# Optimization experiments

Hardware: AMD Instinct MI355X
Metric: run time of the kernel (lower is better)

## Reference

```python
import jax, jax.numpy as jnp
import numpy as np

IN_CAPS, IN_DIM, OUT_CAPS, OUT_DIM = 2048, 8, 32, 16
NUM_ROUTING = 3
EPS = 1e-9


def squash(s):
    # s: [..., out_dim]
    s2 = jnp.sum(s * s, axis=-1, keepdims=True)
    return (s2 / (1.0 + s2)) * (s / jnp.sqrt(s2 + EPS))


def setup_inputs() -> dict:
    key = jax.random.key(0)
    kx, kw = jax.random.split(key)
    x = jax.random.normal(kx, (64, IN_CAPS, IN_DIM), dtype=jnp.float32)
    W = jax.random.normal(kw, (1, IN_CAPS, OUT_CAPS, OUT_DIM, IN_DIM), dtype=jnp.float32) * 0.01
    return {"x": x, "W": W}


def reference(x, W):
    # u_hat[b,i,o,j] = sum_d W[0,i,o,j,d] * x[b,i,d]
    u_hat = jnp.einsum('iojd,bid->bioj', W[0], x)  # [B, in_caps, out_caps, out_dim]
    b_ij = jnp.zeros(u_hat.shape[:3], dtype=u_hat.dtype)  # [B, in_caps, out_caps]
    v_j = None
    for r in range(NUM_ROUTING):
        c_ij = jax.nn.softmax(b_ij, axis=2)[..., None]  # [B, in, out, 1]
        s_j = jnp.sum(c_ij * u_hat, axis=1)             # [B, out, out_dim]
        v_j = squash(s_j)
        if r < NUM_ROUTING - 1:
            b_ij = b_ij + jnp.einsum('bioj,boj->bio', u_hat, v_j)
    return v_j
```

## Files before the change

kernel.cpp:

```cpp
#include <hip/hip_runtime.h>
#include <math.h>


#define IC 2048
#define ID 8
#define OC 32
#define OD 16
#define B_N 64
#define S_ELEMS (B_N * OC * OD)
#define IB 16
#define ISTR (IC / IB)
#define BPB 16
#define BG (B_N / BPB)

__device__ __forceinline__ void gll16(const float4* g, float4* l)
{
    __builtin_amdgcn_global_load_lds(
        (const __attribute__((address_space(1))) void*)g,
        (__attribute__((address_space(3))) void*)l,
        16, 0, 0);
}

template <int CTRL>
__device__ __forceinline__ float dpp_add(float x)
{
    union { float f; int i; } a, b;
    a.f = x;
    b.i = __builtin_amdgcn_update_dpp(0, a.i, CTRL, 0xF, 0xF, true);
    return x + b.f;
}


template <int FIRST>
__launch_bounds__(256, 2)
__global__ void caps_pass(const float* __restrict__ Wg,
                          const float* __restrict__ xg,
                          const float* __restrict__ vs,
                          float* __restrict__ part)
{
    __shared__ float4 Wl[4][1024];
    __shared__ float4 xs[BPB * 32];

    const int tid  = threadIdx.x;
    const int lane = tid & 63;
    const int w    = tid >> 6;
    const int o    = lane & 31;
    const int jh   = lane >> 5;

    const int is   = blockIdx.x & (ISTR - 1);
    const int bg   = blockIdx.x >> 7;
    const int bblk = bg * BPB;
    const int ig0  = is * IB;

    const float4* wq = (const float4*)Wg;
    const float4* xq = (const float4*)xg;

    float4 va[4], vb[4];
    if (!FIRST) {
#pragma unroll
        for (int n = 0; n < 4; ++n) {
            const float* vp =
                vs + (size_t)(bblk + w * 4 + n) * (OC * OD) + o * OD + jh * 8;
            va[n] = ((const float4*)vp)[0];
            vb[n] = ((const float4*)vp)[1];
        }
    }

    float acc[4][8];
#pragma unroll
    for (int n = 0; n < 4; ++n)
#pragma unroll
        for (int jj = 0; jj < 8; ++jj) acc[n][jj] = 0.0f;

    auto stage = [&](int t) {
        const size_t wb0 = (size_t)(ig0 + t) * 1024;
        float4* dst = Wl[t & 3];
#pragma unroll
        for (int s = 0; s < 4; ++s) {
            const int D = s * 256 + tid;
            const int orow = D >> 5;
            const int f = orow * 32 + ((D & 31) ^ orow);
            gll16(wq + wb0 + f, dst + D);
        }
    };

    stage(0);
    stage(1);
    {
#pragma unroll
        for (int q = 0; q < 2; ++q) {
            const int s = q * 256 + tid;
            const int b = s >> 5;
            const int r = s & 31;
            gll16(xq + ((size_t)(bblk + b) * IC + ig0) * 2 + r, &xs[s]);
        }
    }

    auto compute = [&](int il) {
        float4 wA[8], wB[8];
        const float4* buf = Wl[il & 3];
        const int row = o * 32;
#pragma unroll
        for (int jj = 0; jj < 8; ++jj) {
            const int ca = (jh * 16 + jj * 2) ^ o;
            wA[jj] = buf[row + ca];
            wB[jj] = buf[row + (ca ^ 1)];
        }

#pragma unroll
        for (int n = 0; n < 4; ++n) {
            const float4 xa = xs[(w * 4 + n) * 32 + il * 2];
            const float4 xb = xs[(w * 4 + n) * 32 + il * 2 + 1];
            float u[8];
#pragma unroll
            for (int jj = 0; jj < 8; ++jj) {
                float t = wA[jj].x * xa.x;
                t = fmaf(wA[jj].y, xa.y, t);
                t = fmaf(wA[jj].z, xa.z, t);
                t = fmaf(wA[jj].w, xa.w, t);
                t = fmaf(wB[jj].x, xb.x, t);
                t = fmaf(wB[jj].y, xb.y, t);
                t = fmaf(wB[jj].z, xb.z, t);
                t = fmaf(wB[jj].w, xb.w, t);
                u[jj] = t;
            }
            float cc;
            if (FIRST) {
                cc = 1.0f;
            } else {
                float bp = u[0] * va[n].x;
                bp = fmaf(u[1], va[n].y, bp);
                bp = fmaf(u[2], va[n].z, bp);
                bp = fmaf(u[3], va[n].w, bp);
                bp = fmaf(u[4], vb[n].x, bp);
                bp = fmaf(u[5], vb[n].y, bp);
                bp = fmaf(u[6], vb[n].z, bp);
                bp = fmaf(u[7], vb[n].w, bp);
                bp += __shfl_xor(bp, 32);
                const float e = __expf(bp);
                float t = dpp_add<0xB1>(e);
                t = dpp_add<0x4E>(t);
                t = dpp_add<0x124>(t);
                t = dpp_add<0x128>(t);
                const float se = t + __shfl_xor(t, 16);
                cc = e * __builtin_amdgcn_rcpf(se);
            }
#pragma unroll
            for (int jj = 0; jj < 8; ++jj)
                acc[n][jj] = fmaf(cc, u[jj], acc[n][jj]);
        }
    };

    for (int il = 0; il < IB - 2; ++il) {
        stage(il + 2);
        asm volatile("s_waitcnt vmcnt(8)" ::: "memory");
        __builtin_amdgcn_s_barrier();
        compute(il);
    }
    asm volatile("s_waitcnt vmcnt(4)" ::: "memory");
    __builtin_amdgcn_s_barrier();
    compute(IB - 2);
    asm volatile("s_waitcnt vmcnt(0)" ::: "memory");
    __builtin_amdgcn_s_barrier();
    compute(IB - 1);

    const float scale = FIRST ? (1.0f / 32.0f) : 1.0f;
#pragma unroll
    for (int n = 0; n < 4; ++n) {
        float* dst = part + (size_t)is * S_ELEMS
                   + (size_t)(bblk + w * 4 + n) * (OC * OD) + o * OD + jh * 8;
        float4 lo = {acc[n][0] * scale, acc[n][1] * scale,
                     acc[n][2] * scale, acc[n][3] * scale};
        float4 hi = {acc[n][4] * scale, acc[n][5] * scale,
                     acc[n][6] * scale, acc[n][7] * scale};
        ((float4*)dst)[0] = lo;
        ((float4*)dst)[1] = hi;
    }
}

template <int MODE>
__launch_bounds__(256, 4)
__global__ void caps_reduce(const float* __restrict__ part,
                            float* __restrict__ vsum,
                            float* __restrict__ out)
{
    __shared__ float red[4][64];
    const int tid  = threadIdx.x;
    const int w    = tid >> 6;
    const int lane = tid & 63;
    const int e0   = blockIdx.x * 64;

    float s = 0.0f;
#pragma unroll 8
    for (int k = w; k < ISTR; k += 4)
        s += part[(size_t)k * S_ELEMS + e0 + lane];
    red[w][lane] = s;
    __syncthreads();

    if (tid < 64) {
        const float t = red[0][tid] + red[1][tid] + red[2][tid] + red[3][tid];
        float s2 = t * t;
        s2 += __shfl_xor(s2, 1);
        s2 += __shfl_xor(s2, 2);
        s2 += __shfl_xor(s2, 4);
        s2 += __shfl_xor(s2, 8);
        const float v = t * (s2 / ((1.0f + s2) * sqrtf(s2 + 1e-9f)));
        const int e = e0 + tid;
        if (MODE == 0)      vsum[e] = v;
        else if (MODE == 1) vsum[e] += v;
        else                out[e] = v;
    }
}

extern "C" void kernel_launch(void* const* d_in, const int* in_sizes, int n_in,
                              void* d_out, int out_size, void* d_ws, size_t ws_size,
                              hipStream_t stream)
{
    const float* x = (const float*)d_in[0];
    const float* W = (const float*)d_in[1];
    float* out = (float*)d_out;

    float* part = (float*)d_ws;
    float* vsum = part + (size_t)ISTR * S_ELEMS;

    const dim3 gP(BG * ISTR);
    const dim3 bP(256);
    const dim3 gR(S_ELEMS / 64);
    const dim3 bR(256);

    caps_pass<1><<<gP, bP, 0, stream>>>(W, x, nullptr, part);
    caps_reduce<0><<<gR, bR, 0, stream>>>(part, vsum, out);
    caps_pass<0><<<gP, bP, 0, stream>>>(W, x, vsum, part);
    caps_reduce<1><<<gR, bR, 0, stream>>>(part, vsum, out);
    caps_pass<0><<<gP, bP, 0, stream>>>(W, x, vsum, part);
    caps_reduce<2><<<gR, bR, 0, stream>>>(part, vsum, out);
}
```

Before: 170.2 us.

## Fuse all routing passes and reductions into one persistent kernel with grid barriers

Merges the three routing passes and three reduction kernels into a single kernel launch. Atomic-counter grid barriers separate each pass from its reduction, which removes five launch gaps and the kernel boundaries between them. The W pipeline shrinks from a 4-deep async ring to double buffering with __syncthreads, which may expose more load latency. The design assumes all 512 blocks are co-resident (2 per CU over 256 CUs); without that the barrier deadlocks. It also adds a memset launch per call.

New measurement: 537.2 us. +215.7%, slower.

```diff
diff --git a/kernel.cpp b/kernel.cpp
--- a/kernel.cpp
+++ b/kernel.cpp
@@ -12,6 +12,7 @@
 #define ISTR (IC / IB)
 #define BPB 16
 #define BG (B_N / BPB)
+#define NBLK (BG * ISTR)
 
 __device__ __forceinline__ void gll16(const float4* g, float4* l)
 {
@@ -30,16 +31,44 @@
     return x + b.f;
 }
 
-
-template <int FIRST>
+__device__ __forceinline__ void gridbar(unsigned* cnt, unsigned* gen)
+{
+    __syncthreads();
+    if (threadIdx.x == 0) {
+        const unsigned g =
+            __hip_atomic_load(gen, __ATOMIC_RELAXED, __HIP_MEMORY_SCOPE_AGENT);
+        const unsigned a =
+            __hip_atomic_fetch_add(cnt, 1u, __ATOMIC_ACQ_REL,
+                                   __HIP_MEMORY_SCOPE_AGENT);
+        if (a == NBLK - 1) {
+            __hip_atomic_store(cnt, 0u, __ATOMIC_RELAXED,
+                               __HIP_MEMORY_SCOPE_AGENT);
+            __hip_atomic_fetch_add(gen, 1u, __ATOMIC_RELEASE,
+                                   __HIP_MEMORY_SCOPE_AGENT);
+        } else {
+            while (__hip_atomic_load(gen, __ATOMIC_ACQUIRE,
+                                     __HIP_MEMORY_SCOPE_AGENT) == g)
+                __builtin_amdgcn_s_sleep(2);
+        }
+    }
+    __syncthreads();
+}
+
+
 __launch_bounds__(256, 2)
-__global__ void caps_pass(const float* __restrict__ Wg,
-                          const float* __restrict__ xg,
-                          const float* __restrict__ vs,
-                          float* __restrict__ part)
-{
-    __shared__ float4 Wl[4][1024];
-    __shared__ float4 xs[BPB * 32];
+__global__ void caps_fused(const float* __restrict__ Wg,
+                           const float* __restrict__ xg,
+                           float* __restrict__ part,
+                           float* __restrict__ vsum,
+                           float* __restrict__ out,
+                           unsigned* __restrict__ bar)
+{
+    __shared__ float4 Wl[2][1024];
+    __shared__ float4 xs[BPB * 2 * IB];
+    __shared__ float red[4][64];
+
+    unsigned* cnt = bar;
+    unsigned* gen = bar + 1;
 
     const int tid  = threadIdx.x;
     const int lane = tid & 63;
@@ -51,164 +80,148 @@
     const int bg   = blockIdx.x >> 7;
     const int bblk = bg * BPB;
     const int ig0  = is * IB;
+    const int e0   = blockIdx.x * 64;
 
     const float4* wq = (const float4*)Wg;
     const float4* xq = (const float4*)xg;
 
-    float4 va[4], vb[4];
-    if (!FIRST) {
-#pragma unroll
-        for (int n = 0; n < 4; ++n) {
-            const float* vp =
-                vs + (size_t)(bblk + w * 4 + n) * (OC * OD) + o * OD + jh * 8;
-            va[n] = ((const float4*)vp)[0];
-            vb[n] = ((const float4*)vp)[1];
-        }
+#pragma unroll
+    for (int q = 0; q < 2; ++q) {
+        const int s = q * 256 + tid;
+        const int b = s >> 5;
+        const int rr = s & 31;
+        gll16(xq + ((size_t)(bblk + b) * IC + ig0) * 2 + rr, &xs[s]);
     }
 
-    float acc[4][8];
-#pragma unroll
-    for (int n = 0; n < 4; ++n)
-#pragma unroll
-        for (int jj = 0; jj < 8; ++jj) acc[n][jj] = 0.0f;
-
-    auto stage = [&](int t) {
+    auto stage = [&](int t, int parity) {
         const size_t wb0 = (size_t)(ig0 + t) * 1024;
-        float4* dst = Wl[t & 3];
-#pragma unroll
-        for (int s = 0; s < 4; ++s) {
-            const int D = s * 256 + tid;
+        float4* dst = Wl[parity];
+#pragma unroll
+        for (int s4 = 0; s4 < 4; ++s4) {
+            const int D = s4 * 256 + tid;
             const int orow = D >> 5;
             const int f = orow * 32 + ((D & 31) ^ orow);
             gll16(wq + wb0 + f, dst + D);
         }
     };
 
-    stage(0);
-    stage(1);
-    {
-#pragma unroll
-        for (int q = 0; q < 2; ++q) {
-            const int s = q * 256 + tid;
-            const int b = s >> 5;
-            const int r = s & 31;
-            gll16(xq + ((size_t)(bblk + b) * IC + ig0) * 2 + r, &xs[s]);
-        }
-    }
-
-    auto compute = [&](int il) {
-        float4 wA[8], wB[8];
-        const float4* buf = Wl[il & 3];
-        const int row = o * 32;
-#pragma unroll
-        for (int jj = 0; jj < 8; ++jj) {
-            const int ca = (jh * 16 + jj * 2) ^ o;
-            wA[jj] = buf[row + ca];
-            wB[jj] = buf[row + (ca ^ 1)];
-        }
-
+    for (int r = 0; r < 3; ++r) {
+        float4 va[4], vb[4];
+        if (r) {
+#pragma unroll
+            for (int n = 0; n < 4; ++n) {
+                const float* vp = vsum + (size_t)(bblk + w * 4 + n) * (OC * OD)
+                                + o * OD + jh * 8;
+                va[n] = ((const float4*)vp)[0];
+                vb[n] = ((const float4*)vp)[1];
+            }
+        }
+
+        float acc[4][8];
+#pragma unroll
+        for (int n = 0; n < 4; ++n)
+#pragma unroll
+            for (int jj = 0; jj < 8; ++jj) acc[n][jj] = 0.0f;
+
+        stage(0, 0);
+
+        for (int il = 0; il < IB; ++il) {
+            const int p = il & 1;
+            __syncthreads();
+
+            if (il + 1 < IB) stage(il + 1, p ^ 1);
+
+            float4 wA[8], wB[8];
+            const int row = o * 32;
+#pragma unroll
+            for (int jj = 0; jj < 8; ++jj) {
+                const int ca = (jh * 16 + jj * 2) ^ o;
+                wA[jj] = Wl[p][row + ca];
+                wB[jj] = Wl[p][row + (ca ^ 1)];
+            }
+
+#pragma unroll
+            for (int n = 0; n < 4; ++n) {
+                const float4 xa = xs[(w * 4 + n) * 32 + il * 2];
+                const float4 xb = xs[(w * 4 + n) * 32 + il * 2 + 1];
+                float u[8];
+#pragma unroll
+                for (int jj = 0; jj < 8; ++jj) {
+                    float t = wA[jj].x * xa.x;
+                    t = fmaf(wA[jj].y, xa.y, t);
+                    t = fmaf(wA[jj].z, xa.z, t);
+                    t = fmaf(wA[jj].w, xa.w, t);
+                    t = fmaf(wB[jj].x, xb.x, t);
+                    t = fmaf(wB[jj].y, xb.y, t);
+                    t = fmaf(wB[jj].z, xb.z, t);
+                    t = fmaf(wB[jj].w, xb.w, t);
+                    u[jj] = t;
+                }
+                float cc;
+                if (r == 0) {
+                    cc = 1.0f;
+                } else {
+                    float bp = u[0] * va[n].x;
+                    bp = fmaf(u[1], va[n].y, bp);
+                    bp = fmaf(u[2], va[n].z, bp);
+                    bp = fmaf(u[3], va[n].w, bp);
+                    bp = fmaf(u[4], vb[n].x, bp);
+                    bp = fmaf(u[5], vb[n].y, bp);
+                    bp = fmaf(u[6], vb[n].z, bp);
+                    bp = fmaf(u[7], vb[n].w, bp);
+                    bp += __shfl_xor(bp, 32);
+                    const float e = __expf(bp);
+                    float t = dpp_add<0xB1>(e);
+                    t = dpp_add<0x4E>(t);
+                    t = dpp_add<0x124>(t);
+                    t = dpp_add<0x128>(t);
+                    const float se = t + __shfl_xor(t, 16);
+                    cc = e * __builtin_amdgcn_rcpf(se);
+                }
+#pragma unroll
+                for (int jj = 0; jj < 8; ++jj)
+                    acc[n][jj] = fmaf(cc, u[jj], acc[n][jj]);
+            }
+        }
+
+        const float scale = (r == 0) ? (1.0f / 32.0f) : 1.0f;
 #pragma unroll
         for (int n = 0; n < 4; ++n) {
-            const float4 xa = xs[(w * 4 + n) * 32 + il * 2];
-            const float4 xb = xs[(w * 4 + n) * 32 + il * 2 + 1];
-            float u[8];
-#pragma unroll
-            for (int jj = 0; jj < 8; ++jj) {
-                float t = wA[jj].x * xa.x;
-                t = fmaf(wA[jj].y, xa.y, t);
-                t = fmaf(wA[jj].z, xa.z, t);
-                t = fmaf(wA[jj].w, xa.w, t);
-                t = fmaf(wB[jj].x, xb.x, t);
-                t = fmaf(wB[jj].y, xb.y, t);
-                t = fmaf(wB[jj].z, xb.z, t);
-                t = fmaf(wB[jj].w, xb.w, t);
-                u[jj] = t;
-            }
-            float cc;
-            if (FIRST) {
-                cc = 1.0f;
-            } else {
-                float bp = u[0] * va[n].x;
-                bp = fmaf(u[1], va[n].y, bp);
-                bp = fmaf(u[2], va[n].z, bp);
-                bp = fmaf(u[3], va[n].w, bp);
-                bp = fmaf(u[4], vb[n].x, bp);
-                bp = fmaf(u[5], vb[n].y, bp);
-                bp = fmaf(u[6], vb[n].z, bp);
-                bp = fmaf(u[7], vb[n].w, bp);
-                bp += __shfl_xor(bp, 32);
-                const float e = __expf(bp);
-                float t = dpp_add<0xB1>(e);
-                t = dpp_add<0x4E>(t);
-                t = dpp_add<0x124>(t);
-                t = dpp_add<0x128>(t);
-                const float se = t + __shfl_xor(t, 16);
-                cc = e * __builtin_amdgcn_rcpf(se);
-            }
-#pragma unroll
-            for (int jj = 0; jj < 8; ++jj)
-                acc[n][jj] = fmaf(cc, u[jj], acc[n][jj]);
-        }
-    };
-
-    for (int il = 0; il < IB - 2; ++il) {
-        stage(il + 2);
-        asm volatile("s_waitcnt vmcnt(8)" ::: "memory");
-        __builtin_amdgcn_s_barrier();
-        compute(il);
-    }
-    asm volatile("s_waitcnt vmcnt(4)" ::: "memory");
-    __builtin_amdgcn_s_barrier();
-    compute(IB - 2);
-    asm volatile("s_waitcnt vmcnt(0)" ::: "memory");
-    __builtin_amdgcn_s_barrier();
-    compute(IB - 1);
-
-    const float scale = FIRST ? (1.0f / 32.0f) : 1.0f;
-#pragma unroll
-    for (int n = 0; n < 4; ++n) {
-        float* dst = part + (size_t)is * S_ELEMS
-                   + (size_t)(bblk + w * 4 + n) * (OC * OD) + o * OD + jh * 8;
-        float4 lo = {acc[n][0] * scale, acc[n][1] * scale,
-                     acc[n][2] * scale, acc[n][3] * scale};
-        float4 hi = {acc[n][4] * scale, acc[n][5] * scale,
-                     acc[n][6] * scale, acc[n][7] * scale};
-        ((float4*)dst)[0] = lo;
-        ((float4*)dst)[1] = hi;
-    }
-}
-
-template <int MODE>
-__launch_bounds__(256, 4)
-__global__ void caps_reduce(const float* __restrict__ part,
-                            float* __restrict__ vsum,
-                            float* __restrict__ out)
-{
-    __shared__ float red[4][64];
-    const int tid  = threadIdx.x;
-    const int w    = tid >> 6;
-    const int lane = tid & 63;
-    const int e0   = blockIdx.x * 64;
-
-    float s = 0.0f;
+            float* dst = part + (size_t)is * S_ELEMS
+                       + (size_t)(bblk + w * 4 + n) * (OC * OD) + o * OD + jh * 8;
+            float4 lo = {acc[n][0] * scale, acc[n][1] * scale,
+                         acc[n][2] * scale, acc[n][3] * scale};
+            float4 hi = {acc[n][4] * scale, acc[n][5] * scale,
+                         acc[n][6] * scale, acc[n][7] * scale};
+            ((float4*)dst)[0] = lo;
+            ((float4*)dst)[1] = hi;
+        }
+
+        gridbar(cnt, gen);
+
+        float s = 0.0f;
 #pragma unroll 8
-    for (int k = w; k < ISTR; k += 4)
-        s += part[(size_t)k * S_ELEMS + e0 + lane];
-    red[w][lane] = s;
-    __syncthreads();
-
-    if (tid < 64) {
-        const float t = red[0][tid] + red[1][tid] + red[2][tid] + red[3][tid];
-        float s2 = t * t;
-        s2 += __shfl_xor(s2, 1);
-        s2 += __shfl_xor(s2, 2);
-        s2 += __shfl_xor(s2, 4);
-        s2 += __shfl_xor(s2, 8);
-        const float v = t * (s2 / ((1.0f + s2) * sqrtf(s2 + 1e-9f)));
-        const int e = e0 + tid;
-        if (MODE == 0)      vsum[e] = v;
-        else if (MODE == 1) vsum[e] += v;
-        else                out[e] = v;
+        for (int k = w; k < ISTR; k += 4)
+            s += part[(size_t)k * S_ELEMS + e0 + lane];
+        red[w][lane] = s;
+        __syncthreads();
+
+        if (tid < 64) {
+            const float t = red[0][tid] + red[1][tid] + red[2][tid] + red[3][tid];
+            float s2 = t * t;
+            s2 += __shfl_xor(s2, 1);
+            s2 += __shfl_xor(s2, 2);
+            s2 += __shfl_xor(s2, 4);
+            s2 += __shfl_xor(s2, 8);
+            const float v = t * (s2 / ((1.0f + s2) * sqrtf(s2 + 1e-9f)));
+            const int e = e0 + tid;
+            if (r == 0)      vsum[e] = v;
+            else if (r == 1) vsum[e] += v;
+            else             out[e] = v;
+        }
+
+        if (r < 2)
+            gridbar(cnt, gen);
     }
 }
 
@@ -222,16 +235,10 @@
 
     float* part = (float*)d_ws;
     float* vsum = part + (size_t)ISTR * S_ELEMS;
-
-    const dim3 gP(BG * ISTR);
-    const dim3 bP(256);
-    const dim3 gR(S_ELEMS / 64);
-    const dim3 bR(256);
-
-    caps_pass<1><<<gP, bP, 0, stream>>>(W, x, nullptr, part);
-    caps_reduce<0><<<gR, bR, 0, stream>>>(part, vsum, out);
-    caps_pass<0><<<gP, bP, 0, stream>>>(W, x, vsum, part);
-    caps_reduce<1><<<gR, bR, 0, stream>>>(part, vsum, out);
-    caps_pass<0><<<gP, bP, 0, stream>>>(W, x, vsum, part);
-    caps_reduce<2><<<gR, bR, 0, stream>>>(part, vsum, out);
-}
+    unsigned* bar = (unsigned*)(vsum + S_ELEMS);
+
+    hipMemsetAsync(bar, 0, 2 * sizeof(unsigned), stream);
+
+    caps_fused<<<dim3(NBLK), dim3(256), 0, stream>>>(W, x, part, vsum, out,
+                                                     bar);
+}
```
